# Kernel optimization log

Measured on AMD Instinct MI355X. Metric: run time of the kernel, lower is better.

The kernel has to match this reference:

```python
import jax, jax.numpy as jnp
import numpy as np

WS = 8          # window_size
POOL = 7        # int(sqrt(agent_num=49)) -> AdaptiveAvgPool1d output size


def _pool_matrix(L, p):
    """Averaging matrix [L, p] replicating torch AdaptiveAvgPool1d(L -> p)."""
    starts = np.floor(np.arange(p) * L / p).astype(int)
    ends = np.ceil((np.arange(p) + 1) * L / p).astype(int)
    P = np.zeros((L, p), dtype=np.float32)
    for i in range(p):
        P[starts[i]:ends[i], i] = 1.0 / (ends[i] - starts[i])
    return jnp.asarray(P)


def setup_inputs() -> dict:
    key = jax.random.key(0)
    ks = jax.random.split(key, 4)
    B, C, H, W = 8, 96, 192, 192
    s = 1.0 / np.sqrt(C)
    return {
        "x": jax.random.normal(ks[0], (B, C, H, W), jnp.float32),
        "Wv": jax.random.normal(ks[1], (C, C), jnp.float32) * s,
        "bv": jnp.zeros((C,), jnp.float32),
        "Wq": jax.random.normal(ks[2], (C, C), jnp.float32) * s,
        "bq": jnp.zeros((C,), jnp.float32),
        "Wk": jax.random.normal(ks[3], (C, C), jnp.float32) * s,
        "bk": jnp.zeros((C,), jnp.float32),
    }


def _conv1x1(x, Wt, b):
    # Conv2d(dim, dim, 1): weight [out, in]
    return jnp.einsum('bchw,oc->bohw', x, Wt) + b[None, :, None, None]


def reference(x, Wv, bv, Wq, bq, Wk, bk):
    B, C, H, W = x.shape
    ws = WS
    nh, nw = H // ws, W // ws
    L = ws * ws  # tokens per window (64)

    v = _conv1x1(x, Wv, bv)
    q = _conv1x1(x, Wq, bq)
    k = _conv1x1(x, Wk, bk)

    def win(t):  # b c (h dh) (w dw) -> (b h w) (dh dw) c
        t = t.reshape(B, C, nh, ws, nw, ws)
        return t.transpose(0, 2, 4, 3, 5, 1).reshape(B * nh * nw, L, C)

    vw, qw, kw = win(v), win(q), win(k)  # (N, 64, C) each

    # agent tokens: adaptive avg pool over the 64 in-window positions -> 7
    P = _pool_matrix(L, POOL)
    agent = jnp.einsum('nlc,lp->npc', qw, P)  # (N, 7, C)

    # agent attention (attn_drop = 0 -> identity)
    a_attn = jax.nn.softmax(jnp.einsum('npc,nlc->npl', agent, kw), axis=-1)
    agent_v = jnp.einsum('npl,nlc->npc', a_attn, vw)            # (N, 7, C)
    q_attn = jax.nn.softmax(jnp.einsum('nlc,npc->nlp', qw, agent), axis=-1)
    f = jnp.einsum('nlp,npc->nlc', q_attn, agent_v)             # (N, 64, C)

    # (b h w) (dh dw) c -> b c (h dh) (w dw)
    out = f.reshape(B, nh, nw, ws, ws, C).transpose(0, 5, 1, 3, 2, 4)
    return out.reshape(B, C, H, W)
```

## Files before the change

### kernel.cpp

```cpp
#include <hip/hip_runtime.h>


constexpr int C_   = 96;
constexpr int Wimg = 192;
constexpr int HWp  = 192 * 192;
constexpr int NWIN = 24;
constexpr int Pp   = 7;

typedef __attribute__((ext_vector_type(8))) __bf16 bf16x8;
typedef __attribute__((ext_vector_type(4))) __bf16 bf16x4;
typedef __attribute__((ext_vector_type(8))) short  short8;
typedef __attribute__((ext_vector_type(4))) float  f32x4;
union frag_u { short8 s; bf16x8 b; };

constexpr int XWS   = 0;
constexpr int XWLC  = 12288;
constexpr int R1    = 24768;
constexpr int R2    = 31168;
constexpr int QATH  = XWLC;
constexpr int QATL  = XWLC + 2560;
constexpr int AVH   = R2;
constexpr int AVL   = R2 + 3072;
constexpr int BIAS  = 37568;
constexpr int SMEMB = 37632;

constexpr int WS_FRAG_BYTE = 18944 * 4;
constexpr int WS_WV_BYTE   = WS_FRAG_BYTE + 84 * 1024;


__device__ __forceinline__ void bar() {
    asm volatile("s_waitcnt lgkmcnt(0)" ::: "memory");
    __builtin_amdgcn_s_barrier();
}

__device__ __forceinline__ short8 xws_fragA(const unsigned char* S, int mt, int ks, int lane) {
    const int c  = mt * 16 + (lane & 15);
    const int l2 = ks * 64 + ((lane >> 4) << 4);
    return *reinterpret_cast<const short8*>(S + XWS + c * 128 + (l2 ^ ((c & 7) << 4)));
}

__device__ __forceinline__ void put_hilo(unsigned char* S, int hi_off, int lo_off, float v) {
    const __bf16 h = (__bf16)v;
    *reinterpret_cast<__bf16*>(S + hi_off) = h;
    *reinterpret_cast<__bf16*>(S + lo_off) = (__bf16)(v - (float)h);
}


__global__ void precompute_mats(const float* __restrict__ Wq,
                                const float* __restrict__ Wk,
                                float* __restrict__ Mk,
                                float* __restrict__ Mq)
{
    const int c  = blockIdx.x;
    const int cp = threadIdx.x;
    float ak = 0.f, aq = 0.f;
    for (int a = 0; a < C_; ++a) {
        const float wq = Wq[a * C_ + c];
        ak = fmaf(wq, Wk[a * C_ + cp], ak);
        aq = fmaf(wq, Wq[a * C_ + cp], aq);
    }
    Mk[c * C_ + cp] = ak;
    Mq[c * C_ + cp] = aq;
}

__global__ void precompute_vecs(const float* __restrict__ Wq,
                                const float* __restrict__ Wk,
                                const float* __restrict__ bq,
                                const float* __restrict__ bk,
                                float* __restrict__ uk,  float* __restrict__ uq,
                                float* __restrict__ bk2, float* __restrict__ bq2,
                                float* __restrict__ scal)
{
    const int c = threadIdx.x;
    float a_uk = 0.f, a_uq = 0.f, a_bk2 = 0.f, a_bq2 = 0.f;
    for (int a = 0; a < C_; ++a) {
        const float wqc = Wq[a * C_ + c];
        a_uk  = fmaf(wqc, bk[a], a_uk);
        a_uq  = fmaf(wqc, bq[a], a_uq);
        a_bk2 = fmaf(bq[a], Wk[a * C_ + c], a_bk2);
        a_bq2 = fmaf(bq[a], Wq[a * C_ + c], a_bq2);
    }
    uk[c] = a_uk; uq[c] = a_uq; bk2[c] = a_bk2; bq2[c] = a_bq2;
    if (c == 0) {
        float sk = 0.f, sq = 0.f;
        for (int a = 0; a < C_; ++a) { sk += bq[a] * bk[a]; sq += bq[a] * bq[a]; }
        scal[0] = sk; scal[1] = sq;
    }
}

__global__ void precompute_frags(const float* __restrict__ ws,
                                 const float* __restrict__ Wv,
                                 unsigned char* __restrict__ wsb)
{
    const int bid = blockIdx.x, lane = threadIdx.x;
    short8 o;
    if (bid < 84) {
        const int hl = bid & 1, ks = (bid >> 1) % 3, nt = (bid / 6) % 7, mat = bid / 42;
        const float* M = ws + (mat ? 9216 : 0);
        const float* u = ws + (mat ? 18528 : 18432);
        const int col = nt * 16 + (lane & 15);
        #pragma unroll
        for (int j = 0; j < 8; ++j) {
            const int k = ks * 32 + (lane >> 4) * 8 + j;
            const float raw = (col < 96) ? M[k * 96 + col] : ((col == 96) ? u[k] : 0.f);
            const __bf16 hi = (__bf16)raw;
            union { __bf16 h; short s; } cv;
            cv.h = hl ? (__bf16)(raw - (float)hi) : hi;
            o[j] = cv.s;
        }
        *reinterpret_cast<short8*>(wsb + WS_FRAG_BYTE + bid * 1024 + lane * 16) = o;
    } else {
        const int wb = bid - 84;
        const int hl = wb & 1, ks = (wb >> 1) % 3, mt = wb / 6;
        const int row = mt * 16 + (lane & 15);
        #pragma unroll
        for (int j = 0; j < 8; ++j) {
            const int c = ks * 32 + (lane >> 4) * 8 + j;
            const float raw = Wv[row * 96 + c];
            const __bf16 hi = (__bf16)raw;
            union { __bf16 h; short s; } cv;
            cv.h = hl ? (__bf16)(raw - (float)hi) : hi;
            o[j] = cv.s;
        }
        *reinterpret_cast<short8*>(wsb + WS_WV_BYTE + wb * 1024 + lane * 16) = o;
    }
}

#define LOADPAIR(dstH, dstL, tab, slot_h) do {                                               \
    (dstH).s = *reinterpret_cast<const short8*>((tab) + (slot_h) * 1024 + (lane << 4));      \
    (dstL).s = *reinterpret_cast<const short8*>((tab) + ((slot_h) + 1) * 1024 + (lane << 4));\
} while (0)


__global__ __launch_bounds__(256, 4) void camixer_main(
    const float* __restrict__ x,
    const float* __restrict__ bv,
    const float* __restrict__ bk2,
    const float* __restrict__ bq2,
    const float* __restrict__ scal,
    const unsigned char* __restrict__ mfrag,
    const unsigned char* __restrict__ wvfrag,
    float* __restrict__ out)
{
    __shared__ __align__(16) unsigned char S[SMEMB];
    float* Lraw   = (float*)(S + R1);
    float* bias16 = (float*)(S + BIAS);

    const int t = threadIdx.x;
    const int lane = t & 63, w = t >> 6;
    const int wid = ((blockIdx.x & 7) * 576) + (blockIdx.x >> 3);
    const int b  = wid / (NWIN * NWIN);
    const int r  = wid % (NWIN * NWIN);
    const int h0 = (r / NWIN) * 8;
    const int w0 = (r % NWIN) * 8;
    const int base = b * C_ * HWp + h0 * Wimg + w0;
    const float scal0 = scal[0], scal1 = scal[1];
    const short8 zero8 = {0, 0, 0, 0, 0, 0, 0, 0};

    frag_u B0h[3], B0l[3];
    LOADPAIR(B0h[0], B0l[0], mfrag, (w * 3 + 0) * 2);
    LOADPAIR(B0h[1], B0l[1], mfrag, (w * 3 + 1) * 2);
    LOADPAIR(B0h[2], B0l[2], mfrag, (w * 3 + 2) * 2);

    {
        const float4* x4 = reinterpret_cast<const float4*>(x);
        #pragma unroll
        for (int rr = 0; rr < 2; ++rr) {
            const int idx = t + (rr << 8);
            if (idx < 384) {
                const int dw4 = idx & 1;
                const int dh  = (idx >> 1) & 7;
                const int c4  = idx >> 4;
                const int c0 = c4 * 4, l0 = dh * 8 + dw4 * 4;
                __bf16 bf[4][4];
                #pragma unroll
                for (int j = 0; j < 4; ++j) {
                    const float4 v = x4[(base + (c0 + j) * HWp + dh * Wimg + dw4 * 4) >> 2];
                    bf[j][0] = (__bf16)v.x; bf[j][1] = (__bf16)v.y;
                    bf[j][2] = (__bf16)v.z; bf[j][3] = (__bf16)v.w;
                }
                #pragma unroll
                for (int j = 0; j < 4; ++j) {
                    const int c = c0 + j;
                    bf16x4 d = {bf[j][0], bf[j][1], bf[j][2], bf[j][3]};
                    *reinterpret_cast<bf16x4*>(S + XWS + c * 128 + ((l0 * 2) ^ ((c & 7) << 4))) = d;
                }
                #pragma unroll
                for (int i = 0; i < 4; ++i) {
                    const int l = l0 + i;
                    const int s = (c0 >> 5) * 4 + (l >> 4);
                    const int quad = (l & 15) + ((c0 >> 3) & 3) * 16;
                    bf16x4 d = {bf[0][i], bf[1][i], bf[2][i], bf[3][i]};
                    *reinterpret_cast<bf16x4*>(S + XWLC + s * 1040 + quad * 16 + (c0 & 7) * 2) = d;
                }
            }
        }
    }
    bar();

    {
        frag_u PAh[2], PAl[2];
        {
            const int p = lane & 15;
            const __bf16 PH = (__bf16)0.1f;
            const __bf16 PL = (__bf16)(0.1f - (float)PH);
            const int sp = (p < 7) ? ((p << 6) / 7) : 1000;
            #pragma unroll
            for (int ks = 0; ks < 2; ++ks)
                #pragma unroll
                for (int j = 0; j < 8; ++j) {
                    const int l = ks * 32 + (lane >> 4) * 8 + j;
                    const bool in = (l >= sp) && (l < sp + 10);
                    PAh[ks].b[j] = in ? PH : (__bf16)0.f;
                    PAl[ks].b[j] = in ? PL : (__bf16)0.f;
                }
        }
        #pragma unroll
        for (int rnd = 0; rnd < 2; ++rnd) {
            const int nt = rnd ? (4 + w) : w;
            if (rnd == 0 || w < 2) {
                f32x4 acc = {0.f, 0.f, 0.f, 0.f};
                #pragma unroll
                for (int ks = 0; ks < 2; ++ks) {
                    frag_u B;
                    B.s = xws_fragA(S, nt, ks, lane);
                    acc = __builtin_amdgcn_mfma_f32_16x16x32_bf16(PAh[ks].b, B.b, acc, 0, 0, 0);
                    acc = __builtin_amdgcn_mfma_f32_16x16x32_bf16(PAl[ks].b, B.b, acc, 0, 0, 0);
                }
                const int cc = nt * 16 + (lane & 15);
                #pragma unroll
                for (int rr = 0; rr < 4; ++rr) {
                    const int p = (lane >> 4) * 4 + rr;
                    put_hilo(S, R1 + p * 200 + cc * 2, R1 + 3200 + p * 200 + cc * 2, acc[rr]);
                }
            }
        }
    }
    bar();

    {
        frag_u Ah[3], Al[3];
        #pragma unroll
        for (int ks = 0; ks < 3; ++ks) {
            const int off = (lane & 15) * 200 + (ks * 32 + (lane >> 4) * 8) * 2;
            Ah[ks].s = *reinterpret_cast<const short8*>(S + R1 + off);
            Al[ks].s = *reinterpret_cast<const short8*>(S + R1 + 3200 + off);
        }

        #define G0TILE(TT, BH, BL) do {                                               \
            const int tt_ = (TT);                                                     \
            const int mat_ = (tt_ >= 7) ? 1 : 0;                                      \
            const int nt_  = tt_ - 7 * mat_;                                          \
            f32x4 acc = {0.f, 0.f, 0.f, 0.f};                                         \
            acc = __builtin_amdgcn_mfma_f32_16x16x32_bf16(Ah[0].b, BH[0].b, acc, 0,0,0); \
            acc = __builtin_amdgcn_mfma_f32_16x16x32_bf16(Ah[0].b, BL[0].b, acc, 0,0,0); \
            acc = __builtin_amdgcn_mfma_f32_16x16x32_bf16(Al[0].b, BH[0].b, acc, 0,0,0); \
            acc = __builtin_amdgcn_mfma_f32_16x16x32_bf16(Ah[1].b, BH[1].b, acc, 0,0,0); \
            acc = __builtin_amdgcn_mfma_f32_16x16x32_bf16(Ah[1].b, BL[1].b, acc, 0,0,0); \
            acc = __builtin_amdgcn_mfma_f32_16x16x32_bf16(Al[1].b, BH[1].b, acc, 0,0,0); \
            acc = __builtin_amdgcn_mfma_f32_16x16x32_bf16(Ah[2].b, BH[2].b, acc, 0,0,0); \
            acc = __builtin_amdgcn_mfma_f32_16x16x32_bf16(Ah[2].b, BL[2].b, acc, 0,0,0); \
            acc = __builtin_amdgcn_mfma_f32_16x16x32_bf16(Al[2].b, BH[2].b, acc, 0,0,0); \
            const int row0_ = (lane >> 4) * 4;                                        \
            if (nt_ < 6) {                                                            \
                const int cc_ = nt_ * 16 + (lane & 15);                               \
                const float b2v_ = (mat_ ? bq2 : bk2)[cc_];                           \
                _Pragma("unroll")                                                     \
                for (int rr = 0; rr < 4; ++rr) {                                      \
                    const int rw_ = row0_ + rr;                                       \
                    if (rw_ < 8) {                                                    \
                        const int pr_ = rw_ + 8 * mat_;                               \
                        put_hilo(S, R2 + pr_ * 200 + cc_ * 2,                         \
                                 R2 + 3200 + pr_ * 200 + cc_ * 2, acc[rr] + b2v_);    \
                    }                                                                 \
                }                                                                     \
            } else if ((lane & 15) == 0) {                                            \
                _Pragma("unroll")                                                     \
                for (int rr = 0; rr < 4; ++rr) {                                      \
                    const int rw_ = row0_ + rr;                                       \
                    if (rw_ < 8) bias16[rw_ + 8 * mat_] = acc[rr];                    \
                }                                                                     \
            }                                                                         \
        } while (0)

        frag_u B1h[3], B1l[3], B2h[3], B2l[3], B3h[3], B3l[3];
        LOADPAIR(B1h[0], B1l[0], mfrag, ((w + 4) * 3 + 0) * 2);
        LOADPAIR(B1h[1], B1l[1], mfrag, ((w + 4) * 3 + 1) * 2);
        LOADPAIR(B1h[2], B1l[2], mfrag, ((w + 4) * 3 + 2) * 2);
        G0TILE(w, B0h, B0l);
        LOADPAIR(B2h[0], B2l[0], mfrag, ((w + 8) * 3 + 0) * 2);
        LOADPAIR(B2h[1], B2l[1], mfrag, ((w + 8) * 3 + 1) * 2);
        LOADPAIR(B2h[2], B2l[2], mfrag, ((w + 8) * 3 + 2) * 2);
        G0TILE(w + 4, B1h, B1l);
        if (w < 2) {
            LOADPAIR(B3h[0], B3l[0], mfrag, ((w + 12) * 3 + 0) * 2);
            LOADPAIR(B3h[1], B3l[1], mfrag, ((w + 12) * 3 + 1) * 2);
            LOADPAIR(B3h[2], B3l[2], mfrag, ((w + 12) * 3 + 2) * 2);
        }
        G0TILE(w + 8, B2h, B2l);
        if (w < 2) G0TILE(w + 12, B3h, B3l);
        #undef G0TILE
    }
    bar();

    {
        frag_u B[3];
        #pragma unroll
        for (int ks = 0; ks < 3; ++ks)
            B[ks].s = *reinterpret_cast<const short8*>(S + XWLC + (ks * 4 + w) * 1040 + (lane << 4));
        frag_u Ah[3], Al[3];
        #pragma unroll
        for (int ks = 0; ks < 3; ++ks) {
            const int off = (lane & 15) * 200 + (ks * 32 + (lane >> 4) * 8) * 2;
            Ah[ks].s = *reinterpret_cast<const short8*>(S + R2 + off);
            Al[ks].s = *reinterpret_cast<const short8*>(S + R2 + 3200 + off);
        }
        f32x4 acc = {0.f, 0.f, 0.f, 0.f};
        #pragma unroll
        for (int ks = 0; ks < 3; ++ks) {
            acc = __builtin_amdgcn_mfma_f32_16x16x32_bf16(Ah[ks].b, B[ks].b, acc, 0, 0, 0);
            acc = __builtin_amdgcn_mfma_f32_16x16x32_bf16(Al[ks].b, B[ks].b, acc, 0, 0, 0);
        }
        const int colL = w * 16 + (lane & 15);
        #pragma unroll
        for (int rr = 0; rr < 4; ++rr) {
            const int pr = (lane >> 4) * 4 + rr;
            Lraw[pr * 66 + colL] = acc[rr] + bias16[pr] + (pr < 8 ? scal0 : scal1);
        }
    }
    bar();

    if (w < 3) {
        #pragma unroll
        for (int rr = 0; rr < 2; ++rr) {
            const int pp = w + 3 * rr;
            const float v = Lraw[pp * 66 + lane];
            float mx = v;
            #pragma unroll
            for (int off = 32; off; off >>= 1) mx = fmaxf(mx, __shfl_xor(mx, off));
            const float e = __expf(v - mx);
            float s = e;
            #pragma unroll
            for (int off = 32; off; off >>= 1) s += __shfl_xor(s, off);
            const float a = e / s;
            const __bf16 hb = (__bf16)a;
            const __bf16 lb = (__bf16)(a - (float)hb);
            const int ks = lane >> 5;
            const int off_b = ((pp + 16 * ((lane >> 3) & 3)) << 4) + ((lane & 7) << 1);
            *reinterpret_cast<__bf16*>(S + R2 + (ks << 10) + off_b) = hb;
            *reinterpret_cast<__bf16*>(S + R2 + ((2 + ks) << 10) + off_b) = lb;
        }
    } else {
        {
            const int pp = 6;
            const float v = Lraw[pp * 66 + lane];
            float mx = v;
            #pragma unroll
            for (int off = 32; off; off >>= 1) mx = fmaxf(mx, __shfl_xor(mx, off));
            const float e = __expf(v - mx);
            float s = e;
            #pragma unroll
            for (int off = 32; off; off >>= 1) s += __shfl_xor(s, off);
            const float a = e / s;
            const __bf16 hb = (__bf16)a;
            const __bf16 lb = (__bf16)(a - (float)hb);
            const int ks = lane >> 5;
            const int off_b = ((pp + 16 * ((lane >> 3) & 3)) << 4) + ((lane & 7) << 1);
            *reinterpret_cast<__bf16*>(S + R2 + (ks << 10) + off_b) = hb;
            *reinterpret_cast<__bf16*>(S + R2 + ((2 + ks) << 10) + off_b) = lb;
        }
        float vv[Pp];
        float mx = -1e30f;
        #pragma unroll
        for (int p = 0; p < Pp; ++p) { vv[p] = Lraw[(8 + p) * 66 + lane]; mx = fmaxf(mx, vv[p]); }
        float s = 0.f;
        #pragma unroll
        for (int p = 0; p < Pp; ++p) { vv[p] = __expf(vv[p] - mx); s += vv[p]; }
        const float inv = 1.f / s;
        frag_u qh, ql;
        #pragma unroll
        for (int p = 0; p < 8; ++p) {
            const float a = (p < Pp) ? vv[p] * inv : 0.f;
            const __bf16 hb = (__bf16)a;
            qh.b[p] = hb;
            ql.b[p] = (__bf16)(a - (float)hb);
        }
        *reinterpret_cast<short8*>(S + QATH + lane * 40)      = qh.s;
        *reinterpret_cast<short8*>(S + QATH + lane * 40 + 16) = zero8;
        *reinterpret_cast<short8*>(S + QATL + lane * 40)      = ql.s;
        *reinterpret_cast<short8*>(S + QATL + lane * 40 + 16) = zero8;
    }
    bar();

    frag_u V0h[3], V0l[3], V1h[3], V1l[3];
    {
        LOADPAIR(V0h[0], V0l[0], wvfrag, (w * 3 + 0) * 2);
        LOADPAIR(V0h[1], V0l[1], wvfrag, (w * 3 + 1) * 2);
        LOADPAIR(V0h[2], V0l[2], wvfrag, (w * 3 + 2) * 2);
        if (w < 2) {
            LOADPAIR(V1h[0], V1l[0], wvfrag, ((4 + w) * 3 + 0) * 2);
            LOADPAIR(V1h[1], V1l[1], wvfrag, ((4 + w) * 3 + 1) * 2);
            LOADPAIR(V1h[2], V1l[2], wvfrag, ((4 + w) * 3 + 2) * 2);
        }

        frag_u Bh[2], Bl[2];
        #pragma unroll
        for (int ks = 0; ks < 2; ++ks) {
            Bh[ks].s = *reinterpret_cast<const short8*>(S + R2 + (ks << 10) + (lane << 4));
            Bl[ks].s = *reinterpret_cast<const short8*>(S + R2 + ((2 + ks) << 10) + (lane << 4));
        }
        const int mt0 = (w < 2) ? w * 2 : (w + 2);
        const int nmt = (w < 2) ? 2 : 1;
        for (int m = 0; m < nmt; ++m) {
            const int mt = mt0 + m;
            f32x4 acc = {0.f, 0.f, 0.f, 0.f};
            #pragma unroll
            for (int ks = 0; ks < 2; ++ks) {
                frag_u A;
                A.s = xws_fragA(S, mt, ks, lane);
                acc = __builtin_amdgcn_mfma_f32_16x16x32_bf16(A.b, Bh[ks].b, acc, 0, 0, 0);
                acc = __builtin_amdgcn_mfma_f32_16x16x32_bf16(A.b, Bl[ks].b, acc, 0, 0, 0);
            }
            const int p = lane & 15;
            #pragma unroll
            for (int rr = 0; rr < 4; ++rr) {
                const int c = mt * 16 + (lane >> 4) * 4 + rr;
                put_hilo(S, R1 + p * 200 + c * 2, R1 + 3200 + p * 200 + c * 2, acc[rr]);
            }
        }
    }
    bar();

    {
        const bool pok = (lane & 15) < Pp;
        frag_u Bh[3], Bl[3];
        #pragma unroll
        for (int ks = 0; ks < 3; ++ks) {
            const int off = (lane & 15) * 200 + (ks * 32 + (lane >> 4) * 8) * 2;
            Bh[ks].s = pok ? *reinterpret_cast<const short8*>(S + R1 + off)        : zero8;
            Bl[ks].s = pok ? *reinterpret_cast<const short8*>(S + R1 + 3200 + off) : zero8;
        }
        #define G3TILE(MT, VH, VL) do {                                               \
            f32x4 acc = {0.f, 0.f, 0.f, 0.f};                                         \
            acc = __builtin_amdgcn_mfma_f32_16x16x32_bf16(VH[0].b, Bh[0].b, acc, 0,0,0); \
            acc = __builtin_amdgcn_mfma_f32_16x16x32_bf16(VH[0].b, Bl[0].b, acc, 0,0,0); \
            acc = __builtin_amdgcn_mfma_f32_16x16x32_bf16(VL[0].b, Bh[0].b, acc, 0,0,0); \
            acc = __builtin_amdgcn_mfma_f32_16x16x32_bf16(VH[1].b, Bh[1].b, acc, 0,0,0); \
            acc = __builtin_amdgcn_mfma_f32_16x16x32_bf16(VH[1].b, Bl[1].b, acc, 0,0,0); \
            acc = __builtin_amdgcn_mfma_f32_16x16x32_bf16(VL[1].b, Bh[1].b, acc, 0,0,0); \
            acc = __builtin_amdgcn_mfma_f32_16x16x32_bf16(VH[2].b, Bh[2].b, acc, 0,0,0); \
            acc = __builtin_amdgcn_mfma_f32_16x16x32_bf16(VH[2].b, Bl[2].b, acc, 0,0,0); \
            acc = __builtin_amdgcn_mfma_f32_16x16x32_bf16(VL[2].b, Bh[2].b, acc, 0,0,0); \
            _Pragma("unroll")                                                         \
            for (int rr = 0; rr < 4; ++rr) {                                          \
                const int o_ = (MT) * 16 + (lane >> 4) * 4 + rr;                      \
                const float v_ = acc[rr] + bv[o_];                                    \
                put_hilo(S, AVH + o_ * 32 + (lane & 15) * 2,                          \
                         AVL + o_ * 32 + (lane & 15) * 2, v_);                        \
            }                                                                         \
        } while (0)
        G3TILE(w, V0h, V0l);
        if (w < 2) G3TILE(4 + w, V1h, V1l);
        #undef G3TILE
    }
    bar();

    {
        const int kblk = lane >> 4, nlow = lane & 15;
        const int l = w * 16 + nlow;
        frag_u Bh, Bl;
        if (kblk < 2) {
            Bh.s = *reinterpret_cast<const short8*>(S + QATH + l * 40 + kblk * 16);
            Bl.s = *reinterpret_cast<const short8*>(S + QATL + l * 40 + kblk * 16);
        } else { Bh.s = zero8; Bl.s = zero8; }
        const int obase = b * C_ * HWp + (h0 + (l >> 3)) * Wimg + w0 + (l & 7);
        #pragma unroll
        for (int mt = 0; mt < 6; ++mt) {
            frag_u Ah, Al;
            if (kblk < 2) {
                Ah.s = *reinterpret_cast<const short8*>(S + AVH + (mt * 16 + nlow) * 32 + kblk * 16);
                Al.s = *reinterpret_cast<const short8*>(S + AVL + (mt * 16 + nlow) * 32 + kblk * 16);
            } else { Ah.s = zero8; Al.s = zero8; }
            f32x4 acc = {0.f, 0.f, 0.f, 0.f};
            acc = __builtin_amdgcn_mfma_f32_16x16x32_bf16(Ah.b, Bh.b, acc, 0, 0, 0);
            acc = __builtin_amdgcn_mfma_f32_16x16x32_bf16(Ah.b, Bl.b, acc, 0, 0, 0);
            acc = __builtin_amdgcn_mfma_f32_16x16x32_bf16(Al.b, Bh.b, acc, 0, 0, 0);
            #pragma unroll
            for (int rr = 0; rr < 4; ++rr) {
                const int o = mt * 16 + kblk * 4 + rr;
                out[obase + o * HWp] = acc[rr];
            }
        }
    }
}


extern "C" void kernel_launch(void* const* d_in, const int* in_sizes, int n_in,
                              void* d_out, int out_size, void* d_ws, size_t ws_size,
                              hipStream_t stream)
{
    const float* x  = (const float*)d_in[0];
    const float* Wv = (const float*)d_in[1];
    const float* bv = (const float*)d_in[2];
    const float* Wq = (const float*)d_in[3];
    const float* bq = (const float*)d_in[4];
    const float* Wk = (const float*)d_in[5];
    const float* bk = (const float*)d_in[6];
    float* out = (float*)d_out;

    float* ws = (float*)d_ws;
    float* Mk   = ws;
    float* Mq   = ws + 9216;
    float* uk   = ws + 18432;
    float* uq   = ws + 18528;
    float* bk2  = ws + 18624;
    float* bq2  = ws + 18720;
    float* scal = ws + 18816;
    unsigned char* wsb = (unsigned char*)d_ws;

    hipLaunchKernelGGL(precompute_mats, dim3(C_), dim3(C_), 0, stream,
                       Wq, Wk, Mk, Mq);
    hipLaunchKernelGGL(precompute_vecs, dim3(1), dim3(C_), 0, stream,
                       Wq, Wk, bq, bk, uk, uq, bk2, bq2, scal);
    hipLaunchKernelGGL(precompute_frags, dim3(120), dim3(64), 0, stream,
                       ws, Wv, wsb);
    hipLaunchKernelGGL(camixer_main, dim3(8 * NWIN * NWIN), dim3(256), 0, stream,
                       x, bv, bk2, bq2, scal,
                       wsb + WS_FRAG_BYTE, wsb + WS_WV_BYTE, out);
}
```

Measured before the change: 78.27 us.

## Shrink shared memory layout to raise occupancy to five blocks per CU

Drops the second transposed copy of the input window (XWLC) and instead gathers the needed fragments with scalar bf16 LDS reads from the swizzled XWS buffer. The pooled/agent staging is cut to 8 rows, and the regions are re-packed so LDS usage falls from about 37.6KB to 31.3KB, with launch bounds raised to 5 blocks per CU. This trades more, narrower LDS reads for higher occupancy and less LDS write traffic during the load phase, and tighter register limits may cause spills.

```diff
diff --git a/kernel.cpp b/kernel.cpp
--- a/kernel.cpp
+++ b/kernel.cpp
@@ -14,15 +14,18 @@
 union frag_u { short8 s; bf16x8 b; };
 
 constexpr int XWS   = 0;
-constexpr int XWLC  = 12288;
-constexpr int R1    = 24768;
-constexpr int R2    = 31168;
-constexpr int QATH  = XWLC;
-constexpr int QATL  = XWLC + 2560;
-constexpr int AVH   = R2;
-constexpr int AVL   = R2 + 3072;
-constexpr int BIAS  = 37568;
-constexpr int SMEMB = 37632;
+constexpr int XPH   = 12288;
+constexpr int XPL   = 13888;
+constexpr int GKA   = 15488;
+constexpr int GKQH  = GKA;
+constexpr int GKQL  = GKA + 3200;
+constexpr int AVH   = GKA;
+constexpr int AVL   = GKA + 3072;
+constexpr int QATH  = 21888;
+constexpr int QATL  = 24448;
+constexpr int LRAW  = 27008;
+constexpr int BIAS  = 31232;
+constexpr int SMEMB = 31296;
 
 constexpr int WS_FRAG_BYTE = 18944 * 4;
 constexpr int WS_WV_BYTE   = WS_FRAG_BYTE + 84 * 1024;
@@ -132,7 +135,7 @@
 } while (0)
 
 
-__global__ __launch_bounds__(256, 4) void camixer_main(
+__global__ __launch_bounds__(256, 5) void camixer_main(
     const float* __restrict__ x,
     const float* __restrict__ bv,
     const float* __restrict__ bk2,
@@ -143,7 +146,7 @@
     float* __restrict__ out)
 {
     __shared__ __align__(16) unsigned char S[SMEMB];
-    float* Lraw   = (float*)(S + R1);
+    float* Lraw   = (float*)(S + LRAW);
     float* bias16 = (float*)(S + BIAS);
 
     const int t = threadIdx.x;
@@ -172,26 +175,12 @@
                 const int dh  = (idx >> 1) & 7;
                 const int c4  = idx >> 4;
                 const int c0 = c4 * 4, l0 = dh * 8 + dw4 * 4;
-                __bf16 bf[4][4];
-                #pragma unroll
-                for (int j = 0; j < 4; ++j) {
-                    const float4 v = x4[(base + (c0 + j) * HWp + dh * Wimg + dw4 * 4) >> 2];
-                    bf[j][0] = (__bf16)v.x; bf[j][1] = (__bf16)v.y;
-                    bf[j][2] = (__bf16)v.z; bf[j][3] = (__bf16)v.w;
-                }
                 #pragma unroll
                 for (int j = 0; j < 4; ++j) {
                     const int c = c0 + j;
-                    bf16x4 d = {bf[j][0], bf[j][1], bf[j][2], bf[j][3]};
+                    const float4 v = x4[(base + c * HWp + dh * Wimg + dw4 * 4) >> 2];
+                    bf16x4 d = {(__bf16)v.x, (__bf16)v.y, (__bf16)v.z, (__bf16)v.w};
                     *reinterpret_cast<bf16x4*>(S + XWS + c * 128 + ((l0 * 2) ^ ((c & 7) << 4))) = d;
-                }
-                #pragma unroll
-                for (int i = 0; i < 4; ++i) {
-                    const int l = l0 + i;
-                    const int s = (c0 >> 5) * 4 + (l >> 4);
-                    const int quad = (l & 15) + ((c0 >> 3) & 3) * 16;
-                    bf16x4 d = {bf[0][i], bf[1][i], bf[2][i], bf[3][i]};
-                    *reinterpret_cast<bf16x4*>(S + XWLC + s * 1040 + quad * 16 + (c0 & 7) * 2) = d;
                 }
             }
         }
@@ -231,7 +220,8 @@
                 #pragma unroll
                 for (int rr = 0; rr < 4; ++rr) {
                     const int p = (lane >> 4) * 4 + rr;
-                    put_hilo(S, R1 + p * 200 + cc * 2, R1 + 3200 + p * 200 + cc * 2, acc[rr]);
+                    if (p < 8)
+                        put_hilo(S, XPH + p * 200 + cc * 2, XPL + p * 200 + cc * 2, acc[rr]);
                 }
             }
         }
@@ -242,9 +232,9 @@
         frag_u Ah[3], Al[3];
         #pragma unroll
         for (int ks = 0; ks < 3; ++ks) {
-            const int off = (lane & 15) * 200 + (ks * 32 + (lane >> 4) * 8) * 2;
-            Ah[ks].s = *reinterpret_cast<const short8*>(S + R1 + off);
-            Al[ks].s = *reinterpret_cast<const short8*>(S + R1 + 3200 + off);
+            const int off = ((lane & 15) & 7) * 200 + (ks * 32 + (lane >> 4) * 8) * 2;
+            Ah[ks].s = *reinterpret_cast<const short8*>(S + XPH + off);
+            Al[ks].s = *reinterpret_cast<const short8*>(S + XPL + off);
         }
 
         #define G0TILE(TT, BH, BL) do {                                               \
@@ -270,8 +260,8 @@
                     const int rw_ = row0_ + rr;                                       \
                     if (rw_ < 8) {                                                    \
                         const int pr_ = rw_ + 8 * mat_;                               \
-                        put_hilo(S, R2 + pr_ * 200 + cc_ * 2,                         \
-                                 R2 + 3200 + pr_ * 200 + cc_ * 2, acc[rr] + b2v_);    \
+                        put_hilo(S, GKQH + pr_ * 200 + cc_ * 2,                       \
+                                 GKQL + pr_ * 200 + cc_ * 2, acc[rr] + b2v_);         \
                     }                                                                 \
                 }                                                                     \
             } else if ((lane & 15) == 0) {                                            \
@@ -305,15 +295,23 @@
 
     {
         frag_u B[3];
-        #pragma unroll
-        for (int ks = 0; ks < 3; ++ks)
-            B[ks].s = *reinterpret_cast<const short8*>(S + XWLC + (ks * 4 + w) * 1040 + (lane << 4));
+        {
+            const int l2 = (w * 16 + (lane & 15)) * 2;
+            const int kb = (lane >> 4) << 10;
+            #pragma unroll
+            for (int j = 0; j < 8; ++j) {
+                const int aj = kb + j * 128 + (l2 ^ (j << 4));
+                B[0].b[j] = *reinterpret_cast<const __bf16*>(S + XWS + aj);
+                B[1].b[j] = *reinterpret_cast<const __bf16*>(S + XWS + 4096 + aj);
+                B[2].b[j] = *reinterpret_cast<const __bf16*>(S + XWS + 8192 + aj);
+            }
+        }
         frag_u Ah[3], Al[3];
         #pragma unroll
         for (int ks = 0; ks < 3; ++ks) {
             const int off = (lane & 15) * 200 + (ks * 32 + (lane >> 4) * 8) * 2;
-            Ah[ks].s = *reinterpret_cast<const short8*>(S + R2 + off);
-            Al[ks].s = *reinterpret_cast<const short8*>(S + R2 + 3200 + off);
+            Ah[ks].s = *reinterpret_cast<const short8*>(S + GKQH + off);
+            Al[ks].s = *reinterpret_cast<const short8*>(S + GKQL + off);
         }
         f32x4 acc = {0.f, 0.f, 0.f, 0.f};
         #pragma unroll
@@ -347,8 +345,8 @@
             const __bf16 lb = (__bf16)(a - (float)hb);
             const int ks = lane >> 5;
             const int off_b = ((pp + 16 * ((lane >> 3) & 3)) << 4) + ((lane & 7) << 1);
-            *reinterpret_cast<__bf16*>(S + R2 + (ks << 10) + off_b) = hb;
-            *reinterpret_cast<__bf16*>(S + R2 + ((2 + ks) << 10) + off_b) = lb;
+            *reinterpret_cast<__bf16*>(S + GKA + (ks << 10) + off_b) = hb;
+            *reinterpret_cast<__bf16*>(S + GKA + ((2 + ks) << 10) + off_b) = lb;
         }
     } else {
         {
@@ -366,8 +364,8 @@
             const __bf16 lb = (__bf16)(a - (float)hb);
             const int ks = lane >> 5;
             const int off_b = ((pp + 16 * ((lane >> 3) & 3)) << 4) + ((lane & 7) << 1);
-            *reinterpret_cast<__bf16*>(S + R2 + (ks << 10) + off_b) = hb;
-            *reinterpret_cast<__bf16*>(S + R2 + ((2 + ks) << 10) + off_b) = lb;
+            *reinterpret_cast<__bf16*>(S + GKA + (ks << 10) + off_b) = hb;
+            *reinterpret_cast<__bf16*>(S + GKA + ((2 + ks) << 10) + off_b) = lb;
         }
         float vv[Pp];
         float mx = -1e30f;
@@ -406,8 +404,8 @@
         frag_u Bh[2], Bl[2];
         #pragma unroll
         for (int ks = 0; ks < 2; ++ks) {
-            Bh[ks].s = *reinterpret_cast<const short8*>(S + R2 + (ks << 10) + (lane << 4));
-            Bl[ks].s = *reinterpret_cast<const short8*>(S + R2 + ((2 + ks) << 10) + (lane << 4));
+            Bh[ks].s = *reinterpret_cast<const short8*>(S + GKA + (ks << 10) + (lane << 4));
+            Bl[ks].s = *reinterpret_cast<const short8*>(S + GKA + ((2 + ks) << 10) + (lane << 4));
         }
         const int mt0 = (w < 2) ? w * 2 : (w + 2);
         const int nmt = (w < 2) ? 2 : 1;
@@ -422,10 +420,12 @@
                 acc = __builtin_amdgcn_mfma_f32_16x16x32_bf16(A.b, Bl[ks].b, acc, 0, 0, 0);
             }
             const int p = lane & 15;
-            #pragma unroll
-            for (int rr = 0; rr < 4; ++rr) {
-                const int c = mt * 16 + (lane >> 4) * 4 + rr;
-                put_hilo(S, R1 + p * 200 + c * 2, R1 + 3200 + p * 200 + c * 2, acc[rr]);
+            if (p < 8) {
+                #pragma unroll
+                for (int rr = 0; rr < 4; ++rr) {
+                    const int c = mt * 16 + (lane >> 4) * 4 + rr;
+                    put_hilo(S, XPH + p * 200 + c * 2, XPL + p * 200 + c * 2, acc[rr]);
+                }
             }
         }
     }
@@ -436,9 +436,9 @@
         frag_u Bh[3], Bl[3];
         #pragma unroll
         for (int ks = 0; ks < 3; ++ks) {
-            const int off = (lane & 15) * 200 + (ks * 32 + (lane >> 4) * 8) * 2;
-            Bh[ks].s = pok ? *reinterpret_cast<const short8*>(S + R1 + off)        : zero8;
-            Bl[ks].s = pok ? *reinterpret_cast<const short8*>(S + R1 + 3200 + off) : zero8;
+            const int off = ((lane & 15) & 7) * 200 + (ks * 32 + (lane >> 4) * 8) * 2;
+            Bh[ks].s = pok ? *reinterpret_cast<const short8*>(S + XPH + off) : zero8;
+            Bl[ks].s = pok ? *reinterpret_cast<const short8*>(S + XPL + off) : zero8;
         }
         #define G3TILE(MT, VH, VL) do {                                               \
             f32x4 acc = {0.f, 0.f, 0.f, 0.f};                                         \
```

Result: faster. 75.38 us (-3.7%).
